# Optimization experiments

Measured on AMD Instinct MI355X. Metric: run time of the kernel, lower is better.

Reference implementation:

```python
import jax, jax.numpy as jnp
import numpy as np

N = 50000
E = 800000
IN = 256
OUT = 32
H1 = 8
NEG_SLOPE = 0.2


def setup_inputs() -> dict:
    key = jax.random.key(0)
    ks = jax.random.split(key, 12)
    x = jax.random.normal(ks[0], (N, IN), dtype=jnp.float32)
    src = jax.random.randint(ks[1], (E,), 0, N, dtype=jnp.int32)
    dst = jax.random.randint(ks[2], (E,), 0, N, dtype=jnp.int32)
    s1 = 1.0 / np.sqrt(IN)
    s2 = 1.0 / np.sqrt(H1 * OUT)
    # layer 1 (8 heads, residual = Identity since IN == H1*OUT)
    W1 = jax.random.normal(ks[3], (IN, H1 * OUT), dtype=jnp.float32) * s1
    al1 = jax.random.normal(ks[4], (H1, OUT), dtype=jnp.float32) * s1
    ar1 = jax.random.normal(ks[5], (H1, OUT), dtype=jnp.float32) * s1
    b1 = jnp.zeros((H1 * OUT,), dtype=jnp.float32)
    # layer 2 (1 head, residual = Linear since H1*OUT != OUT)
    W2 = jax.random.normal(ks[6], (H1 * OUT, OUT), dtype=jnp.float32) * s2
    al2 = jax.random.normal(ks[7], (1, OUT), dtype=jnp.float32) * s2
    ar2 = jax.random.normal(ks[8], (1, OUT), dtype=jnp.float32) * s2
    resW2 = jax.random.normal(ks[9], (H1 * OUT, OUT), dtype=jnp.float32) * s2
    b2 = jnp.zeros((OUT,), dtype=jnp.float32)
    return {"x": x, "src": src, "dst": dst, "W1": W1, "al1": al1, "ar1": ar1,
            "b1": b1, "W2": W2, "al2": al2, "ar2": ar2, "resW2": resW2, "b2": b2}


def gat_layer(x, src, dst, W, al, ar, bias, heads, out_feats, res_fn):
    # x: (N, in). feat: (N, H, D)
    feat = (x @ W).reshape(N, heads, out_feats)
    el = jnp.sum(feat * al[None], axis=-1)  # (N, H)
    er = jnp.sum(feat * ar[None], axis=-1)  # (N, H)
    e = jax.nn.leaky_relu(el[src] + er[dst], NEG_SLOPE)  # (E, H)
    # edge softmax over incoming edges of each destination node
    emax = jax.ops.segment_max(e, dst, num_segments=N)  # (N, H)
    ee = jnp.exp(e - emax[dst])
    esum = jax.ops.segment_sum(ee, dst, num_segments=N)  # (N, H)
    a = ee / esum[dst]  # (E, H)
    # gather-multiply-scatter-add aggregation
    msg = feat[src] * a[..., None]  # (E, H, D)
    rst = jax.ops.segment_sum(msg, dst, num_segments=N)  # (N, H, D)
    rst = rst + res_fn(x)
    rst = rst + bias.reshape(1, heads, out_feats)
    return rst


def reference(x, src, dst, W1, al1, ar1, b1, W2, al2, ar2, resW2, b2):
    # layer 1: 8 heads, residual Identity (IN == H1*OUT)
    y = gat_layer(x, src, dst, W1, al1, ar1, b1, H1, OUT,
                  lambda h: h.reshape(N, H1, OUT))
    y = jax.nn.relu(y).reshape(N, H1 * OUT)
    # layer 2: 1 head, residual Linear projection
    y = gat_layer(y, src, dst, W2, al2, ar2, b2, 1, OUT,
                  lambda h: (h @ resW2).reshape(N, 1, OUT))
    return y
```

## Files before the change

kernel.cpp:

```cpp
#include <hip/hip_runtime.h>
#include <hip/hip_bf16.h>
#include <hip/hip_fp8.h>

#define N_NODES 50000
#define M_PAD   50048
#define N_EDGES 800000
#define NEG_SLOPE 0.2f

#define EPT 8
#define BKA 391
#define NBUCK 256
#define NPB 196
#define SEGCAP 40
#define GBLK 782
#define APAD 264
#define FUSE1_T (800 + BKA)
#define FUSE2_T (GBLK + NBUCK)

typedef __attribute__((ext_vector_type(8))) short bf16x8;
typedef __attribute__((ext_vector_type(4))) float f32x4;
typedef __attribute__((ext_vector_type(2))) float f32x2;

__device__ __forceinline__ unsigned short f2bf(float f) {
    unsigned u = __float_as_uint(f);
    u += 0x7FFFu + ((u >> 16) & 1u);
    return (unsigned short)(u >> 16);
}
__device__ __forceinline__ float bf2f(unsigned short h) {
    return __uint_as_float(((unsigned)h) << 16);
}

#if __has_builtin(__builtin_amdgcn_cvt_pk_f32_fp8)
__device__ __forceinline__ f32x2 fp8pk_lo(unsigned int p) { return __builtin_amdgcn_cvt_pk_f32_fp8(p, false); }
__device__ __forceinline__ f32x2 fp8pk_hi(unsigned int p) { return __builtin_amdgcn_cvt_pk_f32_fp8(p, true); }
#else
__device__ __forceinline__ float fp82f_s(unsigned char b) {
    __hip_fp8_e4m3 t; t.__x = (__hip_fp8_storage_t)b; return (float)t;
}
__device__ __forceinline__ f32x2 fp8pk_lo(unsigned int p) {
    f32x2 r; r.x = fp82f_s(p & 0xff); r.y = fp82f_s((p >> 8) & 0xff); return r;
}
__device__ __forceinline__ f32x2 fp8pk_hi(unsigned int p) {
    f32x2 r; r.x = fp82f_s((p >> 16) & 0xff); r.y = fp82f_s(p >> 24); return r;
}
#endif

#if __has_builtin(__builtin_amdgcn_cvt_pk_fp8_f32)
__device__ __forceinline__ unsigned int fp8enc2(float a, float b) {
    return (unsigned int)__builtin_amdgcn_cvt_pk_fp8_f32(a, b, 0, false);
}
#else
__device__ __forceinline__ unsigned int fp8enc2(float a, float b) {
    __hip_fp8_e4m3 ta(a), tb(b);
    return (unsigned int)ta.__x | ((unsigned int)tb.__x << 8);
}
#endif


__global__ __launch_bounds__(256) void k_fuse1(const float* __restrict__ W1, const float* __restrict__ W2,
                                               const float* __restrict__ resW2, const float* __restrict__ x,
                                               const int* __restrict__ src, const int* __restrict__ dst,
                                               unsigned short* __restrict__ W1F, unsigned short* __restrict__ W2F,
                                               unsigned short* __restrict__ xb,
                                               uint2* __restrict__ seg, unsigned int* __restrict__ cnt,
                                               unsigned int* __restrict__ btot) {
    int bid = blockIdx.x;
    if (bid >= 800) {
        __shared__ unsigned int lcnt[NBUCK];
        int vb = bid - 800;
        lcnt[threadIdx.x] = 0;
        __syncthreads();
        int base = vb * (256 * EPT) + threadIdx.x;
        int sv[EPT], dv[EPT], bk[EPT], lr[EPT];
        #pragma unroll
        for (int q = 0; q < EPT; ++q) {
            int i = base + q * 256;
            if (i < N_EDGES) { sv[q] = src[i]; dv[q] = dst[i]; }
            else dv[q] = -1;
        }
        #pragma unroll
        for (int q = 0; q < EPT; ++q) {
            if (dv[q] >= 0) {
                bk[q] = (int)((unsigned)dv[q] / NPB);
                lr[q] = atomicAdd(&lcnt[bk[q]], 1u);
            }
        }
        __syncthreads();
        cnt[vb * NBUCK + threadIdx.x] = lcnt[threadIdx.x];
        if (lcnt[threadIdx.x] > 0) atomicAdd(&btot[threadIdx.x], lcnt[threadIdx.x]);
        #pragma unroll
        for (int q = 0; q < EPT; ++q) {
            if (dv[q] >= 0 && lr[q] < SEGCAP) {
                size_t slot = ((size_t)bk[q] * BKA + vb) * SEGCAP + lr[q];
                seg[slot] = make_uint2((unsigned)sv[q], (unsigned)dv[q] - (unsigned)bk[q] * NPB);
            }
        }
        return;
    }
    int flat = bid;
    if (flat < 80) {
        __shared__ unsigned short tile[32][33];
        int bx = flat % 10;
        const float* in;
        int Nn, n0;
        if (bx < 8)      { in = W1;    Nn = 256; n0 = bx * 32; }
        else if (bx == 8){ in = W2;    Nn = 32;  n0 = 0; }
        else             { in = resW2; Nn = 32;  n0 = 0; }
        int k0 = (flat / 10) * 32;
        int tx = threadIdx.x & 31, ty = threadIdx.x >> 5;
        #pragma unroll
        for (int r = 0; r < 4; ++r) {
            int k = k0 + ty + r * 8;
            tile[ty + r * 8][tx] = f2bf(in[(size_t)k * Nn + n0 + tx]);
        }
        __syncthreads();
        #pragma unroll
        for (int r = 0; r < 4; ++r) {
            int n = ty + r * 8;
            unsigned short val = tile[tx][n];
            int col = n0 + n;
            int kk = k0 + tx;
            if (bx < 8) {
                size_t idx = (((size_t)(col >> 4) * 8 + (kk >> 5)) << 9)
                           + ((((kk >> 3) & 3) * 16 + (col & 15)) << 3) + (kk & 7);
                W1F[idx] = val;
            } else {
                int gcol = col + ((bx == 9) ? 32 : 0);
                size_t idx = (((size_t)(gcol >> 4) * 8 + (kk >> 5)) << 9)
                           + ((((kk >> 3) & 3) * 16 + (gcol & 15)) << 3) + (kk & 7);
                W2F[idx] = val;
            }
        }
    } else {
        int xid = flat - 80;
        const size_t NCHUNK = (size_t)M_PAD * 256 / 8;
        for (size_t c = (size_t)xid * 256 + threadIdx.x; c < NCHUNK; c += (size_t)720 * 256) {
            size_t base = c * 8;
            float4 a = make_float4(0.f, 0.f, 0.f, 0.f), b = a;
            if (base < (size_t)N_NODES * 256) {
                a = *(const float4*)(x + base);
                b = *(const float4*)(x + base + 4);
            }
            ushort4 h0, h1;
            h0.x = f2bf(a.x); h0.y = f2bf(a.y); h0.z = f2bf(a.z); h0.w = f2bf(a.w);
            h1.x = f2bf(b.x); h1.y = f2bf(b.y); h1.z = f2bf(b.z); h1.w = f2bf(b.w);
            *(ushort4*)(xb + base) = h0;
            *(ushort4*)(xb + base + 4) = h1;
        }
    }
}


__device__ __forceinline__ void gemm1_body(int gblk,
                                           const unsigned short* __restrict__ xb,
                                           const unsigned short* __restrict__ W1F,
                                           const float* __restrict__ al1, const float* __restrict__ ar1,
                                           unsigned char* __restrict__ Cb8,
                                           float* __restrict__ el1, float* __restrict__ er1) {
    __shared__ unsigned short sA[64 * APAD];
    const int t = threadIdx.x;
    const int bm0 = gblk * 64;
    const int wave = t >> 6, lane = t & 63;
    const int wm = (wave & 1) * 32, wn = (wave >> 1) * 64;
    const int lm = lane & 15, quad = lane >> 4;

    #pragma unroll
    for (int rr = 0; rr < 4; ++rr) {
        int ch = rr * 512 + t;
        int row = ch >> 5, w = ch & 31;
        bf16x8 vv = *(const bf16x8*)(xb + (size_t)(bm0 + row) * 256 + w * 8);
        *(bf16x8*)(sA + row * APAD + w * 8) = vv;
    }
    __syncthreads();

    f32x4 acc[2][4];
    #pragma unroll
    for (int i = 0; i < 2; ++i)
        #pragma unroll
        for (int j = 0; j < 4; ++j)
            #pragma unroll
            for (int r = 0; r < 4; ++r) acc[i][j][r] = 0.f;

    const unsigned short* bp[4];
    #pragma unroll
    for (int i = 0; i < 4; ++i)
        bp[i] = W1F + ((size_t)((wave >> 1) * 4 + i)) * 4096 + lane * 8;
    const unsigned short* ap[2];
    #pragma unroll
    for (int i = 0; i < 2; ++i)
        ap[i] = sA + (wm + i * 16 + lm) * APAD + quad * 8;

    bf16x8 nb[4];
    #pragma unroll
    for (int i = 0; i < 4; ++i) nb[i] = *(const bf16x8*)(bp[i]);

    #pragma unroll
    for (int q = 0; q < 8; ++q) {
        bf16x8 cb[4];
        #pragma unroll
        for (int i = 0; i < 4; ++i) cb[i] = nb[i];
        if (q < 7) {
            #pragma unroll
            for (int i = 0; i < 4; ++i) nb[i] = *(const bf16x8*)(bp[i] + (q + 1) * 512);
        }
        bf16x8 ca[2];
        #pragma unroll
        for (int i = 0; i < 2; ++i) ca[i] = *(const bf16x8*)(ap[i] + q * 32);
        #pragma unroll
        for (int mi = 0; mi < 2; ++mi)
            #pragma unroll
            for (int ni = 0; ni < 4; ++ni)
                acc[mi][ni] = __builtin_amdgcn_mfma_f32_16x16x32_bf16(ca[mi], cb[ni], acc[mi][ni], 0, 0, 0);
    }

    #pragma unroll
    for (int mi = 0; mi < 2; ++mi) {
        #pragma unroll
        for (int ni = 0; ni < 4; ++ni) {
            int col = wn + ni * 16 + lm;
            int row0 = bm0 + wm + mi * 16 + quad * 4;
            unsigned int p01 = fp8enc2(acc[mi][ni][0], acc[mi][ni][1]);
            unsigned int p23 = fp8enc2(acc[mi][ni][2], acc[mi][ni][3]);
            Cb8[(size_t)(row0 + 0) * 256 + col] = (unsigned char)(p01 & 0xff);
            Cb8[(size_t)(row0 + 1) * 256 + col] = (unsigned char)((p01 >> 8) & 0xff);
            Cb8[(size_t)(row0 + 2) * 256 + col] = (unsigned char)(p23 & 0xff);
            Cb8[(size_t)(row0 + 3) * 256 + col] = (unsigned char)((p23 >> 8) & 0xff);
        }
    }
    float alv[4], arv[4];
    #pragma unroll
    for (int ni = 0; ni < 4; ++ni) {
        int colg = wn + ni * 16 + lm;
        alv[ni] = al1[colg];
        arv[ni] = ar1[colg];
    }
    int head0 = wn >> 5;
    #pragma unroll
    for (int gg = 0; gg < 2; ++gg) {
        #pragma unroll
        for (int mi = 0; mi < 2; ++mi) {
            #pragma unroll
            for (int r = 0; r < 4; ++r) {
                float pel = acc[mi][2 * gg][r] * alv[2 * gg] + acc[mi][2 * gg + 1][r] * alv[2 * gg + 1];
                float per = acc[mi][2 * gg][r] * arv[2 * gg] + acc[mi][2 * gg + 1][r] * arv[2 * gg + 1];
                #pragma unroll
                for (int m = 1; m <= 8; m <<= 1) {
                    pel += __shfl_xor(pel, m, 64);
                    per += __shfl_xor(per, m, 64);
                }
                if (lm == 0) {
                    int row = bm0 + wm + mi * 16 + quad * 4 + r;
                    el1[row * 8 + head0 + gg] = pel;
                    er1[row * 8 + head0 + gg] = per;
                }
            }
        }
    }
}


__global__ __launch_bounds__(512) void k_fuse2(const unsigned short* __restrict__ xb,
                                               const unsigned short* __restrict__ W1F,
                                               const float* __restrict__ al1, const float* __restrict__ ar1,
                                               unsigned char* __restrict__ Cb8,
                                               float* __restrict__ el1, float* __restrict__ er1,
                                               const uint2* __restrict__ seg, const unsigned int* __restrict__ cnt,
                                               const unsigned int* __restrict__ btot,
                                               int* __restrict__ rowoff, int* __restrict__ csr_src) {
    int bid = blockIdx.x;
    if (bid < GBLK) {
        gemm1_body(bid, xb, W1F, al1, ar1, Cb8, el1, er1);
        return;
    }
    __shared__ unsigned int hist[NPB];
    __shared__ unsigned int cursor[NPB];
    __shared__ unsigned int red[256];
    int b = bid - GBLK;
    int t = threadIdx.x;
    if (t < NPB) hist[t] = 0;
    if (t < 256) red[t] = (t < b) ? btot[t] : 0;
    __syncthreads();
    #pragma unroll
    for (int off = 128; off > 0; off >>= 1) {
        if (t < off) red[t] += red[t + off];
        __syncthreads();
    }
    unsigned int base = red[0];
    __syncthreads();
    for (int s = t; s < BKA; s += 512) {
        unsigned int c = cnt[s * NBUCK + b];
        const uint2* sp = seg + ((size_t)b * BKA + s) * SEGCAP;
        for (unsigned int j = 0; j < c; ++j) {
            atomicAdd(&hist[sp[j].y], 1u);
        }
    }
    __syncthreads();
    if (t < 256) red[t] = (t < NPB) ? hist[t] : 0;
    __syncthreads();
    for (int off = 1; off < 256; off <<= 1) {
        unsigned int val = (t >= off && t < 256) ? red[t - off] : 0u;
        __syncthreads();
        if (t < 256) red[t] += val;
        __syncthreads();
    }
    if (t < NPB) {
        unsigned int excl = red[t] - hist[t];
        cursor[t] = excl;
        int v = b * NPB + t;
        if (v < N_NODES) rowoff[v] = (int)(base + excl);
    }
    if (b == NBUCK - 1 && t == 0) rowoff[N_NODES] = N_EDGES;
    __syncthreads();
    for (int s = t; s < BKA; s += 512) {
        unsigned int c = cnt[s * NBUCK + b];
        const uint2* sp = seg + ((size_t)b * BKA + s) * SEGCAP;
        for (unsigned int j = 0; j < c; ++j) {
            uint2 eg = sp[j];
            unsigned int r = atomicAdd(&cursor[eg.y], 1u);
            csr_src[base + r] = (int)eg.x;
        }
    }
}


__global__ __launch_bounds__(256) void k_agg1(const unsigned char* __restrict__ feat8,
                                              const float* __restrict__ el1, const float* __restrict__ er1,
                                              const unsigned short* __restrict__ xb, const float* __restrict__ b1,
                                              const int* __restrict__ rowoff, const int* __restrict__ csr_src,
                                              unsigned short* __restrict__ y_b) {
    int v = (blockIdx.x * 256 + threadIdx.x) >> 6;
    int lane = threadIdx.x & 63;
    if (v >= M_PAD) return;
    int c0 = lane * 4;
    if (v >= N_NODES) {
        ushort4 z = {0, 0, 0, 0};
        *(ushort4*)(y_b + (size_t)v * 256 + c0) = z;
        return;
    }
    int h = lane >> 3;
    float er  = er1[v * 8 + h];
    float erc = er1[v * 8 + (lane & 7)];
    float ax = 0.f, ay = 0.f, az = 0.f, aw = 0.f, wsum = 0.f;
    int s = rowoff[v], e = rowoff[v + 1];
    int j = s;
    for (; j + 7 < e; j += 8) {
        int um = csr_src[j + (lane >> 3)];
        float elv = el1[um * 8 + (lane & 7)];
        int u[8];
        #pragma unroll
        for (int q = 0; q < 8; ++q) u[q] = __shfl(um, q * 8);
        unsigned int hv[8];
        #pragma unroll
        for (int q = 0; q < 8; ++q) hv[q] = *(const unsigned int*)(feat8 + (size_t)u[q] * 256 + c0);
        float tq = elv + erc;
        tq = fmaxf(tq, NEG_SLOPE * tq);
        float wv = __expf(tq);
        #pragma unroll
        for (int q = 0; q < 8; ++q) {
            float w = __shfl(wv, q * 8 + h);
            wsum += w;
            f32x2 lo = fp8pk_lo(hv[q]);
            f32x2 hi = fp8pk_hi(hv[q]);
            ax += w * lo.x; ay += w * lo.y; az += w * hi.x; aw += w * hi.y;
        }
    }
    for (; j + 3 < e; j += 4) {
        int u[4];
        #pragma unroll
        for (int q = 0; q < 4; ++q) u[q] = csr_src[j + q];
        float tt[4];
        #pragma unroll
        for (int q = 0; q < 4; ++q) tt[q] = el1[u[q] * 8 + h] + er;
        unsigned int hv[4];
        #pragma unroll
        for (int q = 0; q < 4; ++q) hv[q] = *(const unsigned int*)(feat8 + (size_t)u[q] * 256 + c0);
        #pragma unroll
        for (int q = 0; q < 4; ++q) {
            float tq = fmaxf(tt[q], NEG_SLOPE * tt[q]);
            float w = __expf(tq);
            wsum += w;
            f32x2 lo = fp8pk_lo(hv[q]);
            f32x2 hi = fp8pk_hi(hv[q]);
            ax += w * lo.x; ay += w * lo.y; az += w * hi.x; aw += w * hi.y;
        }
    }
    for (; j < e; ++j) {
        int u = csr_src[j];
        float tt = el1[u * 8 + h] + er;
        unsigned int hh = *(const unsigned int*)(feat8 + (size_t)u * 256 + c0);
        tt = fmaxf(tt, NEG_SLOPE * tt);
        float w = __expf(tt);
        wsum += w;
        f32x2 lo = fp8pk_lo(hh);
        f32x2 hi = fp8pk_hi(hh);
        ax += w * lo.x; ay += w * lo.y; az += w * hi.x; aw += w * hi.y;
    }
    float inv = (e > s) ? 1.f / wsum : 0.f;
    ushort4 rh = *(const ushort4*)(xb + (size_t)v * 256 + c0);
    float4 bb = *(const float4*)(b1 + c0);
    ushort4 o;
    o.x = f2bf(fmaxf(ax * inv + bf2f(rh.x) + bb.x, 0.f));
    o.y = f2bf(fmaxf(ay * inv + bf2f(rh.y) + bb.y, 0.f));
    o.z = f2bf(fmaxf(az * inv + bf2f(rh.z) + bb.z, 0.f));
    o.w = f2bf(fmaxf(aw * inv + bf2f(rh.w) + bb.w, 0.f));
    *(ushort4*)(y_b + (size_t)v * 256 + c0) = o;
}


__global__ __launch_bounds__(256) void k_gemm2f(const unsigned short* __restrict__ Ab,
                                                const unsigned short* __restrict__ W2F,
                                                const float* __restrict__ al2, const float* __restrict__ ar2,
                                                unsigned short* __restrict__ feat2b, float* __restrict__ res2,
                                                float* __restrict__ el2, float* __restrict__ er2) {
    __shared__ unsigned short sA[64 * APAD];
    const int t = threadIdx.x;
    const int bm0 = blockIdx.x * 64;
    const int wave = t >> 6, lane = t & 63;
    const int wm = (wave & 1) * 32, wn = (wave >> 1) * 32;
    const int lm = lane & 15, quad = lane >> 4;

    #pragma unroll
    for (int rr = 0; rr < 8; ++rr) {
        int ch = rr * 256 + t;
        int row = ch >> 5, w = ch & 31;
        bf16x8 vv = *(const bf16x8*)(Ab + (size_t)(bm0 + row) * 256 + w * 8);
        *(bf16x8*)(sA + row * APAD + w * 8) = vv;
    }
    __syncthreads();

    f32x4 acc[2][2];
    #pragma unroll
    for (int i = 0; i < 2; ++i)
        #pragma unroll
        for (int j = 0; j < 2; ++j)
            #pragma unroll
            for (int r = 0; r < 4; ++r) acc[i][j][r] = 0.f;

    const unsigned short* bp[2];
    #pragma unroll
    for (int i = 0; i < 2; ++i)
        bp[i] = W2F + ((size_t)((wn >> 4) + i) * 8) * 512 + lane * 8;
    const unsigned short* ap[2];
    #pragma unroll
    for (int i = 0; i < 2; ++i)
        ap[i] = sA + (wm + i * 16 + lm) * APAD + quad * 8;

    bf16x8 nb[2];
    #pragma unroll
    for (int i = 0; i < 2; ++i) nb[i] = *(const bf16x8*)(bp[i]);

    #pragma unroll
    for (int q = 0; q < 8; ++q) {
        bf16x8 cb[2];
        #pragma unroll
        for (int i = 0; i < 2; ++i) cb[i] = nb[i];
        if (q < 7) {
            #pragma unroll
            for (int i = 0; i < 2; ++i) nb[i] = *(const bf16x8*)(bp[i] + (q + 1) * 512);
        }
        bf16x8 ca[2];
        #pragma unroll
        for (int i = 0; i < 2; ++i) ca[i] = *(const bf16x8*)(ap[i] + q * 32);
        #pragma unroll
        for (int mi = 0; mi < 2; ++mi)
            #pragma unroll
            for (int ni = 0; ni < 2; ++ni)
                acc[mi][ni] = __builtin_amdgcn_mfma_f32_16x16x32_bf16(ca[mi], cb[ni], acc[mi][ni], 0, 0, 0);
    }

    #pragma unroll
    for (int mi = 0; mi < 2; ++mi) {
        #pragma unroll
        for (int ni = 0; ni < 2; ++ni) {
            int col = wn + ni * 16 + lm;
            #pragma unroll
            for (int r = 0; r < 4; ++r) {
                int row = bm0 + wm + mi * 16 + quad * 4 + r;
                float val = acc[mi][ni][r];
                if (col < 32) feat2b[(size_t)row * 32 + col] = f2bf(val);
                else          res2[(size_t)row * 32 + col - 32] = val;
            }
        }
    }
    if (wn == 0) {
        float alv[2], arv[2];
        #pragma unroll
        for (int ni = 0; ni < 2; ++ni) {
            alv[ni] = al2[ni * 16 + lm];
            arv[ni] = ar2[ni * 16 + lm];
        }
        #pragma unroll
        for (int mi = 0; mi < 2; ++mi) {
            #pragma unroll
            for (int r = 0; r < 4; ++r) {
                float pel = acc[mi][0][r] * alv[0] + acc[mi][1][r] * alv[1];
                float per = acc[mi][0][r] * arv[0] + acc[mi][1][r] * arv[1];
                #pragma unroll
                for (int m = 1; m <= 8; m <<= 1) {
                    pel += __shfl_xor(pel, m, 64);
                    per += __shfl_xor(per, m, 64);
                }
                if (lm == 0) {
                    int row = bm0 + wm + mi * 16 + quad * 4 + r;
                    el2[row] = pel;
                    er2[row] = per;
                }
            }
        }
    }
}


__global__ __launch_bounds__(256) void k_agg2(const unsigned short* __restrict__ feat2b,
                                              const float* __restrict__ el2, const float* __restrict__ er2,
                                              const float* __restrict__ res2, const float* __restrict__ b2,
                                              const int* __restrict__ rowoff, const int* __restrict__ csr_src,
                                              float* __restrict__ out) {
    int g = blockIdx.x * 256 + threadIdx.x;
    int v = g >> 5;
    int c = g & 31;
    if (v >= N_NODES) return;
    float er = er2[v];
    float acc = 0.f, wsum = 0.f;
    int s = rowoff[v], e = rowoff[v + 1];
    int j = s;
    for (; j + 3 < e; j += 4) {
        int u[4];
        #pragma unroll
        for (int q = 0; q < 4; ++q) u[q] = csr_src[j + q];
        float tt[4];
        #pragma unroll
        for (int q = 0; q < 4; ++q) tt[q] = el2[u[q]] + er;
        unsigned short fv[4];
        #pragma unroll
        for (int q = 0; q < 4; ++q) fv[q] = feat2b[(size_t)u[q] * 32 + c];
        #pragma unroll
        for (int q = 0; q < 4; ++q) {
            float tq = fmaxf(tt[q], NEG_SLOPE * tt[q]);
            float w = __expf(tq);
            wsum += w;
            acc += w * bf2f(fv[q]);
        }
    }
    for (; j < e; ++j) {
        int u = csr_src[j];
        float t = el2[u] + er;
        t = fmaxf(t, NEG_SLOPE * t);
        float w = __expf(t);
        wsum += w;
        acc += w * bf2f(feat2b[(size_t)u * 32 + c]);
    }
    float inv = (e > s) ? 1.f / wsum : 0.f;
    out[(size_t)v * 32 + c] = acc * inv + res2[(size_t)v * 32 + c] + b2[c];
}


extern "C" void kernel_launch(void* const* d_in, const int* in_sizes, int n_in,
                              void* d_out, int out_size, void* d_ws, size_t ws_size,
                              hipStream_t stream) {
    const float* x     = (const float*)d_in[0];
    const int*   src   = (const int*)d_in[1];
    const int*   dst   = (const int*)d_in[2];
    const float* W1    = (const float*)d_in[3];
    const float* al1   = (const float*)d_in[4];
    const float* ar1   = (const float*)d_in[5];
    const float* b1    = (const float*)d_in[6];
    const float* W2    = (const float*)d_in[7];
    const float* al2   = (const float*)d_in[8];
    const float* ar2   = (const float*)d_in[9];
    const float* resW2 = (const float*)d_in[10];
    const float* b2    = (const float*)d_in[11];
    float* out = (float*)d_out;

    char* ws = (char*)d_ws;
    size_t off = 0;
    auto alloc = [&](size_t bytes) {
        void* p = ws + off;
        off += (bytes + 255) & ~(size_t)255;
        return p;
    };
    unsigned short* xb     = (unsigned short*)alloc((size_t)M_PAD * 256 * 2);
    unsigned char*  feat8  = (unsigned char*)alloc((size_t)M_PAD * 256);
    unsigned short* y_b    = (unsigned short*)alloc((size_t)M_PAD * 256 * 2);
    unsigned short* W1F    = (unsigned short*)alloc((size_t)256 * 256 * 2);
    unsigned short* W2F    = (unsigned short*)alloc((size_t)64 * 256 * 2);
    unsigned short* feat2b = (unsigned short*)alloc((size_t)M_PAD * 32 * 2);
    float* res2   = (float*)alloc((size_t)M_PAD * 32 * 4);
    float* el1    = (float*)alloc((size_t)M_PAD * 8 * 4);
    float* er1    = (float*)alloc((size_t)M_PAD * 8 * 4);
    float* el2    = (float*)alloc((size_t)M_PAD * 4);
    float* er2    = (float*)alloc((size_t)M_PAD * 4);
    int*   rowoff = (int*)alloc((size_t)(N_NODES + 1) * 4);
    int*   csr    = (int*)alloc((size_t)N_EDGES * 4);
    uint2* seg    = (uint2*)alloc((size_t)NBUCK * BKA * SEGCAP * 8);
    unsigned int* cnt  = (unsigned int*)alloc((size_t)BKA * NBUCK * 4);
    unsigned int* btot = (unsigned int*)alloc((size_t)NBUCK * 4);
    (void)ws_size;

    hipMemsetAsync(btot, 0, (size_t)NBUCK * 4, stream);

    k_fuse1<<<FUSE1_T, 256, 0, stream>>>(W1, W2, resW2, x, src, dst, W1F, W2F, xb, seg, cnt, btot);

    k_fuse2<<<FUSE2_T, 512, 0, stream>>>(xb, W1F, al1, ar1, feat8, el1, er1, seg, cnt, btot, rowoff, csr);

    k_agg1<<<(M_PAD * 64) / 256, 256, 0, stream>>>(feat8, el1, er1, xb, b1, rowoff, csr, y_b);

    k_gemm2f<<<M_PAD / 64, 256, 0, stream>>>(y_b, W2F, al2, ar2, feat2b, res2, el2, er2);
    k_agg2<<<(N_NODES * 32) / 256, 256, 0, stream>>>(feat2b, el2, er2, res2, b2, rowoff, csr, out);
}
```

Before: 237.5 us.

## Use one wavefront per node in layer-2 aggregation with shuffled edge weights

The layer-2 aggregation kernel now gives each destination node a full 64-lane wavefront instead of 32 lanes, with the two halves handling alternating edges and a final cross-half reduction. Edge indices and attention weights are computed cooperatively, 16 or 8 edges at once, and broadcast with shuffles, so each lane no longer recomputes the exp and reloads csr/el2 for every edge. This is meant to raise memory-level parallelism on the gather and remove redundant transcendental work. In exchange it launches twice as many threads, adds shuffle overhead, and leaves lanes idle on low-degree nodes.

```diff
diff --git a/kernel.cpp b/kernel.cpp
--- a/kernel.cpp
+++ b/kernel.cpp
@@ -516,42 +516,57 @@
                                               const float* __restrict__ res2, const float* __restrict__ b2,
                                               const int* __restrict__ rowoff, const int* __restrict__ csr_src,
                                               float* __restrict__ out) {
-    int g = blockIdx.x * 256 + threadIdx.x;
-    int v = g >> 5;
-    int c = g & 31;
+    int v = (blockIdx.x * 256 + threadIdx.x) >> 6;
+    int lane = threadIdx.x & 63;
     if (v >= N_NODES) return;
+    int c = lane & 31;
+    int half = lane >> 5;
     float er = er2[v];
     float acc = 0.f, wsum = 0.f;
     int s = rowoff[v], e = rowoff[v + 1];
     int j = s;
-    for (; j + 3 < e; j += 4) {
-        int u[4];
-        #pragma unroll
-        for (int q = 0; q < 4; ++q) u[q] = csr_src[j + q];
-        float tt[4];
-        #pragma unroll
-        for (int q = 0; q < 4; ++q) tt[q] = el2[u[q]] + er;
-        unsigned short fv[4];
-        #pragma unroll
-        for (int q = 0; q < 4; ++q) fv[q] = feat2b[(size_t)u[q] * 32 + c];
-        #pragma unroll
-        for (int q = 0; q < 4; ++q) {
-            float tq = fmaxf(tt[q], NEG_SLOPE * tt[q]);
-            float w = __expf(tq);
+    for (; j + 15 < e; j += 16) {
+        int um = csr_src[j + (lane & 15)];
+        float tq = el2[um] + er;
+        tq = fmaxf(tq, NEG_SLOPE * tq);
+        float wv = __expf(tq);
+        #pragma unroll
+        for (int qq = 0; qq < 8; ++qq) {
+            int edge = 2 * qq + half;
+            int u = __shfl(um, edge);
+            float w = __shfl(wv, edge);
             wsum += w;
-            acc += w * bf2f(fv[q]);
-        }
-    }
-    for (; j < e; ++j) {
-        int u = csr_src[j];
-        float t = el2[u] + er;
-        t = fmaxf(t, NEG_SLOPE * t);
-        float w = __expf(t);
+            acc += w * bf2f(feat2b[(size_t)u * 32 + c]);
+        }
+    }
+    for (; j + 7 < e; j += 8) {
+        int um = csr_src[j + (lane & 7)];
+        float tq = el2[um] + er;
+        tq = fmaxf(tq, NEG_SLOPE * tq);
+        float wv = __expf(tq);
+        #pragma unroll
+        for (int qq = 0; qq < 4; ++qq) {
+            int edge = 2 * qq + half;
+            int u = __shfl(um, edge);
+            float w = __shfl(wv, edge);
+            wsum += w;
+            acc += w * bf2f(feat2b[(size_t)u * 32 + c]);
+        }
+    }
+    for (int k = half; j + k < e; k += 2) {
+        int u = csr_src[j + k];
+        float tt = el2[u] + er;
+        tt = fmaxf(tt, NEG_SLOPE * tt);
+        float w = __expf(tt);
         wsum += w;
         acc += w * bf2f(feat2b[(size_t)u * 32 + c]);
     }
-    float inv = (e > s) ? 1.f / wsum : 0.f;
-    out[(size_t)v * 32 + c] = acc * inv + res2[(size_t)v * 32 + c] + b2[c];
+    acc  += __shfl_xor(acc, 32, 64);
+    wsum += __shfl_xor(wsum, 32, 64);
+    if (lane < 32) {
+        float inv = (e > s) ? 1.f / wsum : 0.f;
+        out[(size_t)v * 32 + c] = acc * inv + res2[(size_t)v * 32 + c] + b2[c];
+    }
 }
 
 
@@ -606,5 +621,5 @@
     k_agg1<<<(M_PAD * 64) / 256, 256, 0, stream>>>(feat8, el1, er1, xb, b1, rowoff, csr, y_b);
 
     k_gemm2f<<<M_PAD / 64, 256, 0, stream>>>(y_b, W2F, al2, ar2, feat2b, res2, el2, er2);
-    k_agg2<<<(N_NODES * 32) / 256, 256, 0, stream>>>(feat2b, el2, er2, res2, b2, rowoff, csr, out);
-}
+    k_agg2<<<(N_NODES * 64) / 256, 256, 0, stream>>>(feat2b, el2, er2, res2, b2, rowoff, csr, out);
+}
```

Measured after the change: 241.3 us. Within noise of the previous version (+1.6%).
